# Kernel tuning notes

Measured on AMD Instinct MI355X. Metric: run time of the kernel, lower is better.

Reference implementation:

```python
import jax, jax.numpy as jnp
import numpy as np

NUM_ENTITIES = 100000
NUM_TIMES = 10000
D = 512
DB = 768
NUM_REL = 200
NUM_BASES = 4
N_NODES = 30000
N_EDGES = 200000
B = 128
P_ENT = 64
P_TIME = 32
T_UNIQ = 2000


def setup_inputs() -> dict:
    key = jax.random.key(0)
    ks = jax.random.split(key, 32)
    n = jax.random.normal
    ri = jax.random.randint
    inp = {}
    # learned params
    inp['emb'] = n(ks[0], (NUM_ENTITIES + NUM_TIMES, D), jnp.float32) * 0.05
    sc = 1.0 / np.sqrt(D)
    inp['basis1'] = n(ks[1], (NUM_BASES, D, D), jnp.float32) * sc
    inp['att1'] = n(ks[2], (NUM_REL, NUM_BASES), jnp.float32) * 0.5
    inp['root1'] = n(ks[3], (D, D), jnp.float32) * sc
    inp['bias1'] = jnp.zeros((D,), jnp.float32)
    inp['basis2'] = n(ks[4], (NUM_BASES, D, D), jnp.float32) * sc
    inp['att2'] = n(ks[5], (NUM_REL, NUM_BASES), jnp.float32) * 0.5
    inp['root2'] = n(ks[6], (D, D), jnp.float32) * sc
    inp['bias2'] = jnp.zeros((D,), jnp.float32)
    sb = 1.0 / np.sqrt(DB)
    inp['W_lin'] = n(ks[7], (DB, D), jnp.float32) * sb
    inp['b_lin'] = jnp.zeros((D,), jnp.float32)
    inp['W_attn'] = n(ks[8], (DB, D), jnp.float32) * sb
    inp['b_attn'] = jnp.zeros((D,), jnp.float32)
    inp['W_prob'] = n(ks[9], (DB, 1), jnp.float32) * sb
    inp['b_prob'] = jnp.zeros((1,), jnp.float32)
    # forward tensor args
    inp['ques_emb_bert'] = n(ks[10], (B, DB), jnp.float32)
    inp['x_idx'] = ri(ks[11], (N_NODES,), 0, NUM_ENTITIES, jnp.int32)
    inp['edge_index'] = ri(ks[12], (2, N_EDGES), 0, N_NODES, jnp.int32)
    inp['edge_type'] = ri(ks[13], (N_EDGES,), 0, NUM_REL, jnp.int32)
    inp['start_time'] = ri(ks[14], (N_EDGES,), 0, NUM_TIMES, jnp.int32)
    inp['end_time'] = ri(ks[15], (N_EDGES,), 0, NUM_TIMES, jnp.int32)
    inp['edge_batch_idx'] = jnp.sort(ri(ks[16], (N_EDGES,), 0, B, jnp.int32))
    inp['edge_norm'] = jax.random.uniform(ks[17], (N_EDGES,), jnp.float32)
    inp['uniq_times'] = ri(ks[18], (T_UNIQ,), 0, NUM_TIMES, jnp.int32)
    # padded index vectors: positions >= count point at the appended zero row
    ent_counts = ri(ks[19], (B,), 1, P_ENT + 1, jnp.int32)
    time_counts = ri(ks[20], (B,), 1, P_TIME + 1, jnp.int32)
    pe = ri(ks[21], (B, P_ENT), 0, N_NODES, jnp.int32)
    pt = ri(ks[22], (B, P_TIME), 0, T_UNIQ, jnp.int32)
    inp['padded_ent'] = jnp.where(jnp.arange(P_ENT)[None, :] < ent_counts[:, None], pe, N_NODES)
    inp['padded_time'] = jnp.where(jnp.arange(P_TIME)[None, :] < time_counts[:, None], pt, T_UNIQ)
    inp['ent_counts'] = ent_counts
    inp['time_counts'] = time_counts
    return inp


def rgcn_layer(x, basis, att, root, bias, src, dst, etype, st_emb, et_emb, q_t, edge_norm):
    # basis decomposition: project all nodes through each basis once. [N, NB, D]
    xb = jnp.einsum('ni,bio->nbo', x, basis)
    coeff = att[etype]                                 # [E, NB]
    msg = jnp.einsum('eb,ebd->ed', coeff, xb[src])     # [E, D]
    # time gate: question-time embedding vs edge interval midpoint embedding
    gate = jax.nn.sigmoid(jnp.sum(q_t * 0.5 * (st_emb + et_emb), axis=-1))  # [E]
    msg = msg * (gate * edge_norm)[:, None]
    agg = jax.ops.segment_sum(msg, dst, num_segments=N_NODES)
    return agg + x @ root + bias


def reference(emb, basis1, att1, root1, bias1, basis2, att2, root2, bias2,
              W_lin, b_lin, W_attn, b_attn, W_prob, b_prob,
              ques_emb_bert, x_idx, edge_index, edge_type, start_time, end_time,
              edge_batch_idx, edge_norm, uniq_times, padded_ent, padded_time,
              ent_counts, time_counts):
    question_embedding = ques_emb_bert @ W_lin + b_lin                  # [B, D]
    time_for_edge_attn = (ques_emb_bert @ W_attn + b_attn)[edge_batch_idx]  # [E, D]
    st_emb = emb[start_time + NUM_ENTITIES]
    et_emb = emb[end_time + NUM_ENTITIES]
    x = emb[x_idx]                                                      # [N, D]
    src, dst = edge_index[0], edge_index[1]
    h = jax.nn.relu(rgcn_layer(x, basis1, att1, root1, bias1, src, dst, edge_type,
                               st_emb, et_emb, time_for_edge_attn, edge_norm))
    # dropout is identity in eval mode
    h = rgcn_layer(h, basis2, att2, root2, bias2, src, dst, edge_type,
                   st_emb, et_emb, time_for_edge_attn, edge_norm)       # [N, D]
    subgraph_time_emb = emb[uniq_times + NUM_ENTITIES]                  # [T_u, D]
    zero = jnp.zeros((1, D), h.dtype)
    ent_w_zeros = jnp.concatenate([h, zero], axis=0)
    time_w_zeros = jnp.concatenate([subgraph_time_emb, zero], axis=0)
    pooled_ent = jnp.sum(ent_w_zeros[padded_ent], axis=1) / ent_counts[:, None].astype(h.dtype)
    pooled_time = jnp.sum(time_w_zeros[padded_time], axis=1) / time_counts[:, None].astype(h.dtype)
    p_ent = jax.nn.sigmoid(ques_emb_bert @ W_prob + b_prob)             # [B, 1]
    pred = (question_embedding + pooled_ent * p_ent + pooled_time * (1.0 - p_ent)) / 3.0
    # batched cosine similarity against full entity+time vocab
    pred_n = pred / jnp.maximum(jnp.linalg.norm(pred, axis=-1, keepdims=True), 1e-8)
    emb_n = emb / jnp.maximum(jnp.linalg.norm(emb, axis=-1, keepdims=True), 1e-8)
    score = pred_n @ emb_n.T                                            # [B, V]
    return score * 30.0
```

## Files before the change

kernel.cpp:

```cpp
#include <hip/hip_runtime.h>

#define NUM_ENT   100000
#define NTIMES    10000
#define DD        512
#define DB        768
#define NREL      200
#define NBAS      4
#define NN        30000
#define NEDGE     200000
#define BATCH     128
#define PENT      64
#define PTIME     32
#define TUNIQ     2000
#define V_TOT     110000
#define V_PAD     110208
#define VCONV     6888
#define M_PAD2    30208
#define KL        2560
#define KT_L      80
#define KT_E      16
#define PACKB_BLKS 1280
#define GATH_BLKS  7500

typedef __attribute__((ext_vector_type(8))) short s8v;
typedef __attribute__((ext_vector_type(4))) float f4v;

__device__ __forceinline__ unsigned short f2bf(float x){
  unsigned int u = __builtin_bit_cast(unsigned int, x);
  u += 0x7fffu + ((u >> 16) & 1u);
  return (unsigned short)(u >> 16);
}
__device__ __forceinline__ float bf2f(unsigned short h){
  unsigned int u = ((unsigned int)h) << 16;
  return __builtin_bit_cast(float, u);
}

__device__ __forceinline__ void gload16(const void* g, void* l){
  __builtin_amdgcn_global_load_lds(
      (const __attribute__((address_space(1))) void*)g,
      (__attribute__((address_space(3))) void*)l, 16, 0, 0);
}


__global__ __launch_bounds__(256) void k_prep(const float* __restrict__ emb,
    const float* __restrict__ basis1, const float* __restrict__ root1,
    const float* __restrict__ basis2, const float* __restrict__ root2,
    const int* __restrict__ x_idx,
    unsigned short* __restrict__ Eb, float* __restrict__ invn,
    unsigned short* __restrict__ Bt1, unsigned short* __restrict__ Bt2,
    unsigned short* __restrict__ Az){
  int bid = blockIdx.x;
  int wid = threadIdx.x >> 6, lane = threadIdx.x & 63;
  if (bid < VCONV){
    #pragma unroll
    for (int i = 0; i < 4; ++i){
      int row = bid * 16 + wid * 4 + i;
      s8v o;
      float ss = 0.f;
      if (row < V_TOT){
        const float4* p = reinterpret_cast<const float4*>(emb + (size_t)row * DD + lane * 8);
        float4 v0 = p[0], v1 = p[1];
        ss = v0.x*v0.x + v0.y*v0.y + v0.z*v0.z + v0.w*v0.w
           + v1.x*v1.x + v1.y*v1.y + v1.z*v1.z + v1.w*v1.w;
        o[0] = (short)f2bf(v0.x); o[1] = (short)f2bf(v0.y);
        o[2] = (short)f2bf(v0.z); o[3] = (short)f2bf(v0.w);
        o[4] = (short)f2bf(v1.x); o[5] = (short)f2bf(v1.y);
        o[6] = (short)f2bf(v1.z); o[7] = (short)f2bf(v1.w);
      } else {
        #pragma unroll
        for (int j = 0; j < 8; ++j) o[j] = 0;
      }
      *reinterpret_cast<s8v*>(Eb + (size_t)row * 512 + lane * 8) = o;
      ss += __shfl_xor(ss, 1);  ss += __shfl_xor(ss, 2);  ss += __shfl_xor(ss, 4);
      ss += __shfl_xor(ss, 8);  ss += __shfl_xor(ss, 16); ss += __shfl_xor(ss, 32);
      if (lane == 0)
        invn[row] = (row < V_TOT) ? (1.0f / fmaxf(sqrtf(ss), 1e-8f)) : 0.0f;
    }
  } else if (bid < VCONV + PACKB_BLKS){
    int wt = (bid - VCONV) * 4 + wid;
    int set = wt >= 2560;
    int wt2 = wt - set * 2560;
    int colg = wt2 / 320, kc = wt2 - colg * 320;
    const float* basis = set ? basis2 : basis1;
    const float* root  = set ? root2  : root1;
    unsigned short* Bt = set ? Bt2 : Bt1;
    int col = colg * 64 + lane;
    int k0 = kc * 8;
    s8v o;
    #pragma unroll
    for (int j = 0; j < 8; ++j){
      int k = k0 + j;
      float v = (k < 2048) ? basis[(size_t)k * 512 + col] : root[(size_t)(k - 2048) * 512 + col];
      o[j] = (short)f2bf(v);
    }
    *reinterpret_cast<s8v*>(Bt + (size_t)col * KL + k0) = o;
  } else {
    int gb = bid - (VCONV + PACKB_BLKS);
    int w = (int)((gb * 256 + threadIdx.x) >> 6);
    if (w >= NN) return;
    int v = x_idx[w];
    const float4* p = reinterpret_cast<const float4*>(emb + (size_t)v * 512 + lane * 8);
    float4 a = p[0], b = p[1];
    s8v x;
    x[0] = (short)f2bf(a.x); x[1] = (short)f2bf(a.y); x[2] = (short)f2bf(a.z); x[3] = (short)f2bf(a.w);
    x[4] = (short)f2bf(b.x); x[5] = (short)f2bf(b.y); x[6] = (short)f2bf(b.z); x[7] = (short)f2bf(b.w);
    *reinterpret_cast<s8v*>(Az + (size_t)w * KL + 2048 + lane * 8) = x;
  }
}

__global__ __launch_bounds__(256) void k_small2(const float* __restrict__ ques,
    const float* __restrict__ Wl, const float* __restrict__ bl,
    const float* __restrict__ Wa, const float* __restrict__ ba,
    const float* __restrict__ Wp, const float* __restrict__ bp,
    float* __restrict__ qlin, unsigned short* __restrict__ qat,
    float* __restrict__ pent){
  if (blockIdx.x == 32){
    int b = threadIdx.x >> 1, half = threadIdx.x & 1;
    float a = 0.f;
    int k0 = half * 384;
    for (int k = k0; k < k0 + 384; ++k)
      a = fmaf(ques[(size_t)b * DB + k], Wp[k], a);
    a += __shfl_xor(a, 1);
    if (half == 0) pent[b] = 1.f / (1.f + expf(-(a + bp[0])));
    return;
  }
  __shared__ float sq[128 * 96];
  int col = threadIdx.x & 31, bg = threadIdx.x >> 5;
  int c0 = blockIdx.x * 32;
  const float* W = (c0 < 512) ? Wl : Wa;
  int wcol = (c0 & 511) + col;
  float acc[16] = {};
  for (int k0 = 0; k0 < DB; k0 += 96){
    __syncthreads();
    for (int i = threadIdx.x; i < 128 * 96; i += 256){
      int b = i / 96, kk = i - b * 96;
      sq[i] = ques[(size_t)b * DB + k0 + kk];
    }
    __syncthreads();
    for (int kk = 0; kk < 96; kk += 4){
      float w0 = W[(size_t)(k0 + kk + 0) * 512 + wcol];
      float w1 = W[(size_t)(k0 + kk + 1) * 512 + wcol];
      float w2 = W[(size_t)(k0 + kk + 2) * 512 + wcol];
      float w3 = W[(size_t)(k0 + kk + 3) * 512 + wcol];
      #pragma unroll
      for (int bb = 0; bb < 16; ++bb){
        float4 qv = *reinterpret_cast<const float4*>(&sq[(bg * 16 + bb) * 96 + kk]);
        acc[bb] = fmaf(qv.x, w0, fmaf(qv.y, w1, fmaf(qv.z, w2, fmaf(qv.w, w3, acc[bb]))));
      }
    }
  }
  if (c0 < 512){
    #pragma unroll
    for (int bb = 0; bb < 16; ++bb)
      qlin[(size_t)(bg * 16 + bb) * 512 + wcol] = acc[bb] + bl[wcol];
  } else {
    float bb_ = ba[wcol];
    #pragma unroll
    for (int bb = 0; bb < 16; ++bb)
      qat[(size_t)(bg * 16 + bb) * 512 + wcol] = f2bf(acc[bb] + bb_);
  }
}

__global__ __launch_bounds__(256) void k_gemm_m2(
    const unsigned short* __restrict__ qat, const unsigned short* __restrict__ Eb,
    float* __restrict__ outf){
  __shared__ __align__(1024) short sAll[3 * 8192];
  const int Kt = KT_E;
  int tid = threadIdx.x;
  int lane = tid & 63, wid = tid >> 6;
  int wr = wid >> 1, wc = wid & 1;
  int r16 = lane & 15, kq = lane >> 4;
  int rt0 = blockIdx.x * 8;
  int ct0 = blockIdx.y * 8;
  const unsigned short* pA0 = qat + (size_t)((rt0 + 2 * wid) * 16 + r16) * 512 + kq * 8;
  const unsigned short* pA1 = qat + (size_t)((rt0 + 2 * wid + 1) * 16 + r16) * 512 + kq * 8;
  const unsigned short* pB0 = Eb + (size_t)(NUM_ENT + (ct0 + 2 * wid) * 16 + r16) * 512 + kq * 8;
  const unsigned short* pB1 = Eb + (size_t)(NUM_ENT + (ct0 + 2 * wid + 1) * 16 + r16) * 512 + kq * 8;
  int so = 2 * wid * 512;
  f4v acc[4][4] = {};

  auto STAGE = [&](int buf, int kt){
    short* b = &sAll[buf * 8192];
    gload16(pA0 + kt * 32, b + so);
    gload16(pA1 + kt * 32, b + so + 512);
    gload16(pB0 + kt * 32, b + 4096 + so);
    gload16(pB1 + kt * 32, b + 4096 + so + 512);
  };
  auto COMPUTE = [&](int buf){
    const short* base = &sAll[buf * 8192];
    s8v af[4], bfr[4];
    #pragma unroll
    for (int m = 0; m < 4; ++m) af[m] = *reinterpret_cast<const s8v*>(base + (wr * 4 + m) * 512 + lane * 8);
    #pragma unroll
    for (int n = 0; n < 4; ++n) bfr[n] = *reinterpret_cast<const s8v*>(base + 4096 + (wc * 4 + n) * 512 + lane * 8);
    #pragma unroll
    for (int m = 0; m < 4; ++m)
      #pragma unroll
      for (int n = 0; n < 4; ++n)
        acc[m][n] = __builtin_amdgcn_mfma_f32_16x16x32_bf16(af[m], bfr[n], acc[m][n], 0, 0, 0);
  };

  STAGE(0, 0);
  STAGE(1, 1);
  int cb = 0, sb = 2;
  for (int kt = 0; kt < Kt - 2; ++kt){
    STAGE(sb, kt + 2);
    asm volatile("s_waitcnt vmcnt(8)" ::: "memory");
    __builtin_amdgcn_s_barrier();
    __builtin_amdgcn_sched_barrier(0);
    COMPUTE(cb);
    __builtin_amdgcn_s_barrier();
    cb = (cb == 2) ? 0 : cb + 1;
    sb = (sb == 2) ? 0 : sb + 1;
  }
  asm volatile("s_waitcnt vmcnt(4)" ::: "memory");
  __builtin_amdgcn_s_barrier();
  __builtin_amdgcn_sched_barrier(0);
  COMPUTE(cb);
  cb = (cb == 2) ? 0 : cb + 1;
  asm volatile("s_waitcnt vmcnt(0)" ::: "memory");
  __builtin_amdgcn_s_barrier();
  __builtin_amdgcn_sched_barrier(0);
  COMPUTE(cb);

  #pragma unroll
  for (int m = 0; m < 4; ++m)
    #pragma unroll
    for (int n = 0; n < 4; ++n){
      int row0 = rt0 * 16 + (wr * 4 + m) * 16 + ((lane >> 4) * 4);
      int col  = (ct0 + wc * 4 + n) * 16 + (lane & 15);
      #pragma unroll
      for (int r = 0; r < 4; ++r){
        int rr = row0 + r;
        if (col < NTIMES) outf[(size_t)rr * NTIMES + col] = acc[m][n][r];
      }
    }
}

__global__ __launch_bounds__(256, 3) void k_score_p(
    const unsigned short* __restrict__ predb, const unsigned short* __restrict__ Eb,
    const float* __restrict__ invn, float* __restrict__ out){
  __shared__ __align__(1024) short sAll[3 * 8192];
  const int Kt = KT_E;
  int tid = threadIdx.x;
  int lane = tid & 63, wid = tid >> 6;
  int wr = wid >> 1, wc = wid & 1;
  int kq = lane >> 4, r16 = lane & 15;
  int ct0 = blockIdx.x * 8;
  const unsigned short* pA0 = predb + (size_t)(2 * wid * 16 + r16) * 512 + kq * 8;
  const unsigned short* pA1 = predb + (size_t)((2 * wid + 1) * 16 + r16) * 512 + kq * 8;
  const unsigned short* pB0 = Eb + (size_t)((ct0 + 2 * wid) * 16 + r16) * 512 + kq * 8;
  const unsigned short* pB1 = Eb + (size_t)((ct0 + 2 * wid + 1) * 16 + r16) * 512 + kq * 8;
  int so = 2 * wid * 512;
  f4v acc[4][4] = {};

  auto STAGE = [&](int buf, int kt){
    short* b = &sAll[buf * 8192];
    gload16(pA0 + kt * 32, b + so);
    gload16(pA1 + kt * 32, b + so + 512);
    gload16(pB0 + kt * 32, b + 4096 + so);
    gload16(pB1 + kt * 32, b + 4096 + so + 512);
  };
  auto COMPUTE = [&](int buf){
    const short* base = &sAll[buf * 8192];
    s8v af[4], bfr[4];
    #pragma unroll
    for (int m = 0; m < 4; ++m) af[m] = *reinterpret_cast<const s8v*>(base + (wr * 4 + m) * 512 + lane * 8);
    #pragma unroll
    for (int n = 0; n < 4; ++n) bfr[n] = *reinterpret_cast<const s8v*>(base + 4096 + (wc * 4 + n) * 512 + lane * 8);
    #pragma unroll
    for (int m = 0; m < 4; ++m)
      #pragma unroll
      for (int n = 0; n < 4; ++n)
        acc[m][n] = __builtin_amdgcn_mfma_f32_16x16x32_bf16(af[m], bfr[n], acc[m][n], 0, 0, 0);
  };

  STAGE(0, 0);
  STAGE(1, 1);
  int cb = 0, sb = 2;
  for (int kt = 0; kt < Kt - 2; ++kt){
    STAGE(sb, kt + 2);
    asm volatile("s_waitcnt vmcnt(8)" ::: "memory");
    __builtin_amdgcn_s_barrier();
    __builtin_amdgcn_sched_barrier(0);
    COMPUTE(cb);
    __builtin_amdgcn_s_barrier();
    cb = (cb == 2) ? 0 : cb + 1;
    sb = (sb == 2) ? 0 : sb + 1;
  }
  asm volatile("s_waitcnt vmcnt(4)" ::: "memory");
  __builtin_amdgcn_s_barrier();
  __builtin_amdgcn_sched_barrier(0);
  COMPUTE(cb);
  cb = (cb == 2) ? 0 : cb + 1;
  asm volatile("s_waitcnt vmcnt(0)" ::: "memory");
  __builtin_amdgcn_s_barrier();
  __builtin_amdgcn_sched_barrier(0);
  COMPUTE(cb);

  __syncthreads();
  float* scratch = reinterpret_cast<float*>(sAll) + wid * 2176;
  int colg = ct0 * 16 + wc * 64 + r16 * 4;
  bool c_ok = colg < V_TOT;
  float4 inv4 = float4{0.f, 0.f, 0.f, 0.f};
  if (c_ok){
    inv4 = *reinterpret_cast<const float4*>(invn + colg);
    inv4.x *= 30.f; inv4.y *= 30.f; inv4.z *= 30.f; inv4.w *= 30.f;
  }
  #pragma unroll
  for (int p = 0; p < 2; ++p){
    #pragma unroll
    for (int mm = 0; mm < 2; ++mm){
      int m = p * 2 + mm;
      #pragma unroll
      for (int n = 0; n < 4; ++n)
        #pragma unroll
        for (int r = 0; r < 4; ++r)
          scratch[(mm * 16 + kq * 4 + r) * 68 + n * 16 + r16] = acc[m][n][r];
    }
    #pragma unroll
    for (int i = 0; i < 8; ++i){
      int row_r = i * 4 + kq;
      float4 v = *reinterpret_cast<const float4*>(scratch + row_r * 68 + r16 * 4);
      if (c_ok){
        float4 o;
        o.x = v.x * inv4.x; o.y = v.y * inv4.y; o.z = v.z * inv4.z; o.w = v.w * inv4.w;
        int grr = wr * 64 + p * 32 + row_r;
        *reinterpret_cast<float4*>(out + (size_t)grr * V_TOT + colg) = o;
      }
    }
  }
}

template<int MODE>
__global__ __launch_bounds__(512, 2) void k_gemm512(
    const unsigned short* __restrict__ A, const unsigned short* __restrict__ Bt,
    const float* __restrict__ bias, unsigned short* __restrict__ outh,
    unsigned short* __restrict__ Az_h){
  __shared__ __align__(1024) short sAll[3 * 20480];
  const int Kt = KT_L;
  int tid = threadIdx.x;
  int lane = tid & 63, wid = tid >> 6;
  int wr = wid >> 2, wc = wid & 3;
  int r16 = lane & 15, kq = lane >> 4;
  int blk = blockIdx.x;
  const unsigned short* pA = A + (size_t)(blk * 128 + wid * 16 + r16) * KL + kq * 8;
  const unsigned short* pB0 = Bt + (size_t)((wid * 4 + 0) * 16 + r16) * KL + kq * 8;
  const unsigned short* pB1 = Bt + (size_t)((wid * 4 + 1) * 16 + r16) * KL + kq * 8;
  const unsigned short* pB2 = Bt + (size_t)((wid * 4 + 2) * 16 + r16) * KL + kq * 8;
  const unsigned short* pB3 = Bt + (size_t)((wid * 4 + 3) * 16 + r16) * KL + kq * 8;
  int soA = wid * 512;
  int soB = 4096 + wid * 4 * 512;
  f4v acc[4][8] = {};

  auto STAGE = [&](int buf, int kt){
    short* b = &sAll[buf * 20480];
    gload16(pA  + kt * 32, b + soA);
    gload16(pB0 + kt * 32, b + soB);
    gload16(pB1 + kt * 32, b + soB +  512);
    gload16(pB2 + kt * 32, b + soB + 1024);
    gload16(pB3 + kt * 32, b + soB + 1536);
  };
  auto COMPUTE = [&](int buf){
    const short* base = &sAll[buf * 20480];
    s8v af[4], bfr[8];
    #pragma unroll
    for (int m = 0; m < 4; ++m) af[m] = *reinterpret_cast<const s8v*>(base + (wr * 4 + m) * 512 + lane * 8);
    #pragma unroll
    for (int n = 0; n < 8; ++n) bfr[n] = *reinterpret_cast<const s8v*>(base + 4096 + (wc * 8 + n) * 512 + lane * 8);
    __builtin_amdgcn_s_setprio(1);
    #pragma unroll
    for (int m = 0; m < 4; ++m)
      #pragma unroll
      for (int n = 0; n < 8; ++n)
        acc[m][n] = __builtin_amdgcn_mfma_f32_16x16x32_bf16(af[m], bfr[n], acc[m][n], 0, 0, 0);
    __builtin_amdgcn_s_setprio(0);
  };

  STAGE(0, 0);
  STAGE(1, 1);
  int cb = 0, sb = 2;
  for (int kt = 0; kt < Kt - 2; ++kt){
    STAGE(sb, kt + 2);
    asm volatile("s_waitcnt vmcnt(10)" ::: "memory");
    __builtin_amdgcn_s_barrier();
    __builtin_amdgcn_sched_barrier(0);
    COMPUTE(cb);
    __builtin_amdgcn_s_barrier();
    cb = (cb == 2) ? 0 : cb + 1;
    sb = (sb == 2) ? 0 : sb + 1;
  }
  asm volatile("s_waitcnt vmcnt(5)" ::: "memory");
  __builtin_amdgcn_s_barrier();
  __builtin_amdgcn_sched_barrier(0);
  COMPUTE(cb);
  cb = (cb == 2) ? 0 : cb + 1;
  asm volatile("s_waitcnt vmcnt(0)" ::: "memory");
  __builtin_amdgcn_s_barrier();
  __builtin_amdgcn_sched_barrier(0);
  COMPUTE(cb);

  int R0 = blk * 128 + wr * 64 + ((lane >> 4) * 4);
  int C0 = wc * 128 + (lane & 15);
  #pragma unroll
  for (int m = 0; m < 4; ++m)
    #pragma unroll
    for (int r4 = 0; r4 < 4; ++r4){
      int rr = R0 + m * 16 + r4;
      if (rr < NN){
        #pragma unroll
        for (int n = 0; n < 8; ++n){
          int col = C0 + n * 16;
          float v = acc[m][n][r4] + bias[col];
          if constexpr (MODE == 1){
            v = fmaxf(v, 0.f);
            Az_h[(size_t)rr * KL + 2048 + col] = f2bf(v);
          } else {
            outh[(size_t)rr * 512 + col] = f2bf(v);
          }
        }
      }
    }
}

__global__ __launch_bounds__(256) void k_edgeprep(const int* __restrict__ ebatch,
    const int* __restrict__ st, const int* __restrict__ et,
    const float* __restrict__ enorm, const float* __restrict__ M2,
    const int* __restrict__ ei,
    float* __restrict__ we, int* __restrict__ cnt, int* __restrict__ lists){
  int e = blockIdx.x * 256 + threadIdx.x;
  if (e >= NEDGE) return;
  int b = ebatch[e];
  float s = 0.5f * (M2[(size_t)b * NTIMES + st[e]] + M2[(size_t)b * NTIMES + et[e]]);
  we[e] = (1.f / (1.f + expf(-s))) * enorm[e];
  int dst = ei[NEDGE + e];
  int slot = atomicAdd(&cnt[dst], 1);
  if (slot < 64) lists[(size_t)dst * 64 + slot] = e;
}

__global__ __launch_bounds__(256) void k_edge_agg(const unsigned short* __restrict__ xsrc,
    const int* __restrict__ ei, const int* __restrict__ etype,
    const float* __restrict__ we, const float* __restrict__ att,
    const int* __restrict__ cnt, const int* __restrict__ lists,
    unsigned short* __restrict__ Az){
  __shared__ float satt[NREL * NBAS];
  __shared__ int sed[4][64];
  for (int i = threadIdx.x; i < NREL * NBAS; i += 256) satt[i] = att[i];
  int wid = threadIdx.x >> 6, lane = threadIdx.x & 63;
  int n = blockIdx.x * 4 + wid;
  int deg = min(cnt[n], 64);
  int eid = (lane < deg) ? lists[(size_t)n * 64 + lane] : 0x7fffffff;
  int rank = 0;
  for (int j = 0; j < 64; ++j){
    int v = __shfl(eid, j);
    rank += (v < eid) ? 1 : 0;
  }
  __syncthreads();
  if (lane < deg) sed[wid][rank] = eid;
  __syncthreads();
  float acc[NBAS][8] = {};
  if (deg > 0){
    int my_e = sed[wid][(lane < deg) ? lane : 0];
    int my_s = ei[my_e];
    int my_t = etype[my_e];
    float my_w = we[my_e];
    float c0l = my_w * satt[my_t * 4 + 0];
    float c1l = my_w * satt[my_t * 4 + 1];
    float c2l = my_w * satt[my_t * 4 + 2];
    float c3l = my_w * satt[my_t * 4 + 3];
    int s0 = __shfl(my_s, 0);
    s8v xv = *reinterpret_cast<const s8v*>(xsrc + (size_t)s0 * KL + lane * 8);
    for (int j = 0; j < deg; ++j){
      s8v xn = xv;
      if (j + 1 < deg){
        int sn = __shfl(my_s, j + 1);
        xn = *reinterpret_cast<const s8v*>(xsrc + (size_t)sn * KL + lane * 8);
      }
      float c0 = __shfl(c0l, j), c1 = __shfl(c1l, j);
      float c2 = __shfl(c2l, j), c3 = __shfl(c3l, j);
      #pragma unroll
      for (int jj = 0; jj < 8; ++jj){
        float x = bf2f((unsigned short)xv[jj]);
        acc[0][jj] = fmaf(c0, x, acc[0][jj]);
        acc[1][jj] = fmaf(c1, x, acc[1][jj]);
        acc[2][jj] = fmaf(c2, x, acc[2][jj]);
        acc[3][jj] = fmaf(c3, x, acc[3][jj]);
      }
      xv = xn;
    }
  }
  #pragma unroll
  for (int b = 0; b < NBAS; ++b){
    s8v o;
    #pragma unroll
    for (int jj = 0; jj < 8; ++jj) o[jj] = (short)f2bf(acc[b][jj]);
    *reinterpret_cast<s8v*>(Az + (size_t)n * KL + b * 512 + lane * 8) = o;
  }
}

__global__ __launch_bounds__(256) void k_pred(const unsigned short* __restrict__ h2,
    const float* __restrict__ emb, const int* __restrict__ uniq,
    const int* __restrict__ pent_idx, const int* __restrict__ ptime_idx,
    const int* __restrict__ ent_c, const int* __restrict__ time_c,
    const float* __restrict__ qlin, const float* __restrict__ pent,
    unsigned short* __restrict__ predb){
  __shared__ float sacc[4][512];
  int b = blockIdx.x;
  int wid = threadIdx.x >> 6, lane = threadIdx.x & 63;
  float a[8] = {};
  if (wid < 2){
    for (int j = wid * 32; j < wid * 32 + 32; ++j){
      int idx = pent_idx[b * PENT + j];
      if (idx < NN){
        s8v hv = *reinterpret_cast<const s8v*>(h2 + (size_t)idx * 512 + lane * 8);
        #pragma unroll
        for (int jj = 0; jj < 8; ++jj) a[jj] += bf2f((unsigned short)hv[jj]);
      }
    }
  } else {
    for (int j = (wid - 2) * 16; j < (wid - 2) * 16 + 16; ++j){
      int ti = ptime_idx[b * PTIME + j];
      if (ti < TUNIQ){
        const float* p = emb + (size_t)(NUM_ENT + uniq[ti]) * 512 + lane * 8;
        #pragma unroll
        for (int jj = 0; jj < 8; ++jj) a[jj] += p[jj];
      }
    }
  }
  #pragma unroll
  for (int jj = 0; jj < 8; ++jj) sacc[wid][lane * 8 + jj] = a[jj];
  __syncthreads();
  if (wid == 0){
    float ce = 1.f / (float)ent_c[b], ct = 1.f / (float)time_c[b];
    float p = pent[b];
    float pr[8]; float ss = 0.f;
    #pragma unroll
    for (int jj = 0; jj < 8; ++jj){
      int i = lane * 8 + jj;
      float ae = sacc[0][i] + sacc[1][i];
      float at = sacc[2][i] + sacc[3][i];
      float v = (qlin[(size_t)b * 512 + i] + ae * ce * p + at * ct * (1.f - p)) * (1.f / 3.f);
      pr[jj] = v; ss += v * v;
    }
    ss += __shfl_xor(ss, 32); ss += __shfl_xor(ss, 16); ss += __shfl_xor(ss, 8);
    ss += __shfl_xor(ss, 4);  ss += __shfl_xor(ss, 2);  ss += __shfl_xor(ss, 1);
    float inv = 1.f / fmaxf(sqrtf(ss), 1e-8f);
    s8v o;
    #pragma unroll
    for (int jj = 0; jj < 8; ++jj) o[jj] = (short)f2bf(pr[jj] * inv);
    *reinterpret_cast<s8v*>(predb + (size_t)b * 512 + lane * 8) = o;
  }
}

extern "C" void kernel_launch(void* const* d_in, const int* in_sizes, int n_in,
                              void* d_out, int out_size, void* d_ws, size_t ws_size,
                              hipStream_t stream){
  const float* emb    = (const float*)d_in[0];
  const float* basis1 = (const float*)d_in[1];
  const float* att1   = (const float*)d_in[2];
  const float* root1  = (const float*)d_in[3];
  const float* bias1  = (const float*)d_in[4];
  const float* basis2 = (const float*)d_in[5];
  const float* att2   = (const float*)d_in[6];
  const float* root2  = (const float*)d_in[7];
  const float* bias2  = (const float*)d_in[8];
  const float* W_lin  = (const float*)d_in[9];
  const float* b_lin  = (const float*)d_in[10];
  const float* W_attn = (const float*)d_in[11];
  const float* b_attn = (const float*)d_in[12];
  const float* W_prob = (const float*)d_in[13];
  const float* b_prob = (const float*)d_in[14];
  const float* ques   = (const float*)d_in[15];
  const int* x_idx    = (const int*)d_in[16];
  const int* eidx     = (const int*)d_in[17];
  const int* etype    = (const int*)d_in[18];
  const int* stime    = (const int*)d_in[19];
  const int* etime    = (const int*)d_in[20];
  const int* ebatch   = (const int*)d_in[21];
  const float* enorm  = (const float*)d_in[22];
  const int* uniq     = (const int*)d_in[23];
  const int* pent_i   = (const int*)d_in[24];
  const int* ptime_i  = (const int*)d_in[25];
  const int* ent_c    = (const int*)d_in[26];
  const int* time_c   = (const int*)d_in[27];
  float* out = (float*)d_out;

  char* w = (char*)d_ws;
  size_t off = 0;
  auto alloc = [&](size_t bytes)->char*{ char* p = w + off; off += (bytes + 255) & ~(size_t)255; return p; };
  unsigned short* Eb   = (unsigned short*)alloc((size_t)V_PAD * 512 * 2);
  float*          invn = (float*)alloc((size_t)V_PAD * 4);
  unsigned short* Az   = (unsigned short*)alloc((size_t)M_PAD2 * KL * 2);
  unsigned short* Bt1  = (unsigned short*)alloc((size_t)512 * KL * 2);
  unsigned short* Bt2  = (unsigned short*)alloc((size_t)512 * KL * 2);
  unsigned short* h2   = (unsigned short*)alloc((size_t)NN * 512 * 2);
  float* M2    = (float*)alloc((size_t)BATCH * NTIMES * 4);
  float* we    = (float*)alloc((size_t)NEDGE * 4);
  float* qlin  = (float*)alloc((size_t)BATCH * 512 * 4);
  float* pent  = (float*)alloc(1024);
  unsigned short* qat   = (unsigned short*)alloc((size_t)BATCH * 512 * 2);
  unsigned short* predb = (unsigned short*)alloc((size_t)BATCH * 512 * 2);
  int* cnt   = (int*)alloc((size_t)NN * 4);
  int* lists = (int*)alloc((size_t)NN * 64 * 4);
  (void)ws_size; (void)in_sizes; (void)n_in; (void)out_size;

  k_prep<<<VCONV + PACKB_BLKS + GATH_BLKS, 256, 0, stream>>>(
      emb, basis1, root1, basis2, root2, x_idx,
      Eb, invn, Bt1, Bt2, Az);
  k_small2<<<33, 256, 0, stream>>>(ques, W_lin, b_lin, W_attn, b_attn, W_prob, b_prob,
                                   qlin, qat, pent);
  k_gemm_m2<<<dim3(1, 79), 256, 0, stream>>>(qat, Eb, M2);
  hipMemsetAsync(cnt, 0, (size_t)NN * 4, stream);
  k_edgeprep<<<(NEDGE + 255) / 256, 256, 0, stream>>>(ebatch, stime, etime, enorm, M2,
                                                      eidx, we, cnt, lists);
  k_edge_agg<<<NN / 4, 256, 0, stream>>>(Az + 2048, eidx, etype, we, att1, cnt, lists, Az);
  k_gemm512<1><<<236, 512, 0, stream>>>(Az, Bt1, bias1, nullptr, Az);
  k_edge_agg<<<NN / 4, 256, 0, stream>>>(Az + 2048, eidx, etype, we, att2, cnt, lists, Az);
  k_gemm512<2><<<236, 512, 0, stream>>>(Az, Bt2, bias2, h2, nullptr);
  k_pred<<<BATCH, 256, 0, stream>>>(h2, emb, uniq, pent_i, ptime_i, ent_c, time_c,
                                    qlin, pent, predb);
  k_score_p<<<861, 256, 0, stream>>>(predb, Eb, invn, out);
}
```

Before: 669.7 us.

## Retile RGCN layer GEMM to 128x128 tiles with XCD-aware block remap

Replaces the 128x512 output tile GEMM (236 blocks of 512 threads) with a 128x128 tile kernel (944 blocks of 256 threads). Block indices are remapped so that consecutive tiles sharing A rows land on the same XCD, aiming for better L2 reuse. The goal is higher occupancy and better load balance across the 256 CUs, since 236 large blocks underfill the device. The cost is that each A tile is now loaded four times instead of once, and the s_setprio hints are dropped.

New measurement: 726.1 us. 8.4% more time.

```diff
diff --git a/kernel.cpp b/kernel.cpp
--- a/kernel.cpp
+++ b/kernel.cpp
@@ -333,48 +333,45 @@
 }
 
 template<int MODE>
-__global__ __launch_bounds__(512, 2) void k_gemm512(
+__global__ __launch_bounds__(256) void k_gemm128(
     const unsigned short* __restrict__ A, const unsigned short* __restrict__ Bt,
     const float* __restrict__ bias, unsigned short* __restrict__ outh,
     unsigned short* __restrict__ Az_h){
-  __shared__ __align__(1024) short sAll[3 * 20480];
+  __shared__ __align__(1024) short sAll[3 * 8192];
   const int Kt = KT_L;
   int tid = threadIdx.x;
   int lane = tid & 63, wid = tid >> 6;
-  int wr = wid >> 2, wc = wid & 3;
+  int wr = wid >> 1, wc = wid & 1;
   int r16 = lane & 15, kq = lane >> 4;
-  int blk = blockIdx.x;
-  const unsigned short* pA = A + (size_t)(blk * 128 + wid * 16 + r16) * KL + kq * 8;
-  const unsigned short* pB0 = Bt + (size_t)((wid * 4 + 0) * 16 + r16) * KL + kq * 8;
-  const unsigned short* pB1 = Bt + (size_t)((wid * 4 + 1) * 16 + r16) * KL + kq * 8;
-  const unsigned short* pB2 = Bt + (size_t)((wid * 4 + 2) * 16 + r16) * KL + kq * 8;
-  const unsigned short* pB3 = Bt + (size_t)((wid * 4 + 3) * 16 + r16) * KL + kq * 8;
-  int soA = wid * 512;
-  int soB = 4096 + wid * 4 * 512;
-  f4v acc[4][8] = {};
+  int g = blockIdx.x;
+  int ng = (g & 7) * 118 + (g >> 3);
+  int mt = ng >> 2, nt = ng & 3;
+  const unsigned short* pA0 = A + (size_t)(mt * 128 + (wid * 2 + 0) * 16 + r16) * KL + kq * 8;
+  const unsigned short* pA1 = A + (size_t)(mt * 128 + (wid * 2 + 1) * 16 + r16) * KL + kq * 8;
+  const unsigned short* pB0 = Bt + (size_t)(nt * 128 + (wid * 2 + 0) * 16 + r16) * KL + kq * 8;
+  const unsigned short* pB1 = Bt + (size_t)(nt * 128 + (wid * 2 + 1) * 16 + r16) * KL + kq * 8;
+  int so = 2 * wid * 512;
+  f4v acc[4][4] = {};
 
   auto STAGE = [&](int buf, int kt){
-    short* b = &sAll[buf * 20480];
-    gload16(pA  + kt * 32, b + soA);
-    gload16(pB0 + kt * 32, b + soB);
-    gload16(pB1 + kt * 32, b + soB +  512);
-    gload16(pB2 + kt * 32, b + soB + 1024);
-    gload16(pB3 + kt * 32, b + soB + 1536);
+    short* b = &sAll[buf * 8192];
+    gload16(pA0 + kt * 32, b + so);
+    gload16(pA1 + kt * 32, b + so + 512);
+    gload16(pB0 + kt * 32, b + 4096 + so);
+    gload16(pB1 + kt * 32, b + 4096 + so + 512);
   };
   auto COMPUTE = [&](int buf){
-    const short* base = &sAll[buf * 20480];
-    s8v af[4], bfr[8];
+    const short* base = &sAll[buf * 8192];
+    s8v af[4], bfr[4];
     #pragma unroll
     for (int m = 0; m < 4; ++m) af[m] = *reinterpret_cast<const s8v*>(base + (wr * 4 + m) * 512 + lane * 8);
     #pragma unroll
-    for (int n = 0; n < 8; ++n) bfr[n] = *reinterpret_cast<const s8v*>(base + 4096 + (wc * 8 + n) * 512 + lane * 8);
-    __builtin_amdgcn_s_setprio(1);
+    for (int n = 0; n < 4; ++n) bfr[n] = *reinterpret_cast<const s8v*>(base + 4096 + (wc * 4 + n) * 512 + lane * 8);
     #pragma unroll
     for (int m = 0; m < 4; ++m)
       #pragma unroll
-      for (int n = 0; n < 8; ++n)
+      for (int n = 0; n < 4; ++n)
         acc[m][n] = __builtin_amdgcn_mfma_f32_16x16x32_bf16(af[m], bfr[n], acc[m][n], 0, 0, 0);
-    __builtin_amdgcn_s_setprio(0);
   };
 
   STAGE(0, 0);
@@ -382,7 +379,7 @@
   int cb = 0, sb = 2;
   for (int kt = 0; kt < Kt - 2; ++kt){
     STAGE(sb, kt + 2);
-    asm volatile("s_waitcnt vmcnt(10)" ::: "memory");
+    asm volatile("s_waitcnt vmcnt(8)" ::: "memory");
     __builtin_amdgcn_s_barrier();
     __builtin_amdgcn_sched_barrier(0);
     COMPUTE(cb);
@@ -390,7 +387,7 @@
     cb = (cb == 2) ? 0 : cb + 1;
     sb = (sb == 2) ? 0 : sb + 1;
   }
-  asm volatile("s_waitcnt vmcnt(5)" ::: "memory");
+  asm volatile("s_waitcnt vmcnt(4)" ::: "memory");
   __builtin_amdgcn_s_barrier();
   __builtin_amdgcn_sched_barrier(0);
   COMPUTE(cb);
@@ -400,8 +397,8 @@
   __builtin_amdgcn_sched_barrier(0);
   COMPUTE(cb);
 
-  int R0 = blk * 128 + wr * 64 + ((lane >> 4) * 4);
-  int C0 = wc * 128 + (lane & 15);
+  int R0 = mt * 128 + wr * 64 + kq * 4;
+  int C0 = nt * 128 + wc * 64 + r16;
   #pragma unroll
   for (int m = 0; m < 4; ++m)
     #pragma unroll
@@ -409,7 +406,7 @@
       int rr = R0 + m * 16 + r4;
       if (rr < NN){
         #pragma unroll
-        for (int n = 0; n < 8; ++n){
+        for (int n = 0; n < 4; ++n){
           int col = C0 + n * 16;
           float v = acc[m][n][r4] + bias[col];
           if constexpr (MODE == 1){
@@ -614,9 +611,9 @@
   k_edgeprep<<<(NEDGE + 255) / 256, 256, 0, stream>>>(ebatch, stime, etime, enorm, M2,
                                                       eidx, we, cnt, lists);
   k_edge_agg<<<NN / 4, 256, 0, stream>>>(Az + 2048, eidx, etype, we, att1, cnt, lists, Az);
-  k_gemm512<1><<<236, 512, 0, stream>>>(Az, Bt1, bias1, nullptr, Az);
+  k_gemm128<1><<<944, 256, 0, stream>>>(Az, Bt1, bias1, nullptr, Az);
   k_edge_agg<<<NN / 4, 256, 0, stream>>>(Az + 2048, eidx, etype, we, att2, cnt, lists, Az);
-  k_gemm512<2><<<236, 512, 0, stream>>>(Az, Bt2, bias2, h2, nullptr);
+  k_gemm128<2><<<944, 256, 0, stream>>>(Az, Bt2, bias2, h2, nullptr);
   k_pred<<<BATCH, 256, 0, stream>>>(h2, emb, uniq, pent_i, ptime_i, ent_c, time_c,
                                     qlin, pent, predb);
   k_score_p<<<861, 256, 0, stream>>>(predb, Eb, invn, out);
```
